# Optimization experiments

Hardware: AMD Instinct MI355X
Metric: run time of the kernel (lower is better)

## Reference

```python
import jax, jax.numpy as jnp
import numpy as np

N = 16                      # input_dim (state dimension)
EPS = 1e-6
TRIL_R, TRIL_C = np.tril_indices(N)   # 136 lower-triangular slots


def setup_inputs() -> dict:
    key = jax.random.key(0)
    ks = jax.random.split(key, 7)
    B = 131072
    def xavier(k, fan_in, fan_out):
        lim = float(np.sqrt(6.0 / (fan_in + fan_out)))
        return jax.random.uniform(k, (fan_in, fan_out), jnp.float32, -lim, lim)
    return {
        "points": jax.random.normal(ks[0], (B, N), jnp.float32),
        "W0": xavier(ks[1], N, 512),
        "b0": jax.random.normal(ks[2], (512,), jnp.float32) * 0.01,
        "W1": xavier(ks[3], 512, 512),
        "b1": jax.random.normal(ks[4], (512,), jnp.float32) * 0.01,
        "W2": xavier(ks[5], 512, 136),
        "b2": jax.random.normal(ks[6], (136,), jnp.float32) * 0.01,
    }


def reference(points, W0, b0, W1, b1, W2, b2):
    # MLP: tanh, tanh, identity
    h = jnp.tanh(points @ W0 + b0)
    h = jnp.tanh(h @ W1 + b1)
    net = h @ W2 + b2                         # [B, 136] tril entries
    B = points.shape[0]
    # Batched scatter into lower-triangular matrices M: [B, N, N]
    M = jnp.zeros((B, N, N), points.dtype).at[:, TRIL_R, TRIL_C].set(net)
    # x^T (M M^T) x == ||M^T x||^2
    y = jnp.einsum('bij,bi->bj', M, points)   # (M^T x)_j = sum_i M_ij x_i
    vals = jnp.sum(y * y, axis=-1) + EPS * jnp.sum(points * points, axis=-1)
    return vals.reshape(-1, 1)
```

## Files before the change

kernel.cpp:

```cpp
#include <hip/hip_runtime.h>

typedef __bf16 bf16x4 __attribute__((ext_vector_type(4)));
typedef __bf16 bf16x8 __attribute__((ext_vector_type(8)));
typedef float f32x16 __attribute__((ext_vector_type(16)));

#define W0F_OFF 0
#define W1F_OFF 8192
#define W2F_OFF (8192 + 262144)

__global__ void prep_weights(const float* __restrict__ W0,
                             const float* __restrict__ W1,
                             const float* __restrict__ W2,
                             __bf16* __restrict__ ws) {
    const int wave = blockIdx.x * 8 + (threadIdx.x >> 6);
    const int l   = threadIdx.x & 63;
    const int col = l & 31, kh = l >> 5;
    const float* src; int nt, kk, S, nlim;
    if (wave < 16)       { src = W0; nt = wave; kk = 0;          S = 512; nlim = 512; }
    else if (wave < 528) { int r = wave - 16;  src = W1; nt = r >> 5; kk = r & 31; S = 512; nlim = 512; }
    else                 { int r = wave - 528; src = W2; nt = r >> 5; kk = r & 31; S = 136; nlim = 136; }
    const int n  = nt * 32 + col;
    const int k0 = kk * 16 + kh * 8;
    bf16x8 v;
#pragma unroll
    for (int j = 0; j < 8; ++j)
        v[j] = (n < nlim) ? (__bf16)src[(k0 + j) * S + n] : (__bf16)0.0f;
    *(bf16x8*)(ws + wave * 512 + l * 8) = v;
}

__device__ __forceinline__ float fast_tanh(float x) {
#if __has_builtin(__builtin_amdgcn_exp2f)
    float e = __builtin_amdgcn_exp2f(x * 2.885390081777926f);
#else
    float e = exp2f(x * 2.885390081777926f);
#endif
    return 1.0f - 2.0f * __builtin_amdgcn_rcpf(e + 1.0f);
}

#define HSTR 520
#define NSTR 140

__global__ __launch_bounds__(512, 2)
void fused_mlp_quad(const float* __restrict__ points,
                    const float* __restrict__ b0,
                    const float* __restrict__ b1,
                    const float* __restrict__ b2,
                    const __bf16* __restrict__ ws,
                    float* __restrict__ out) {
    __shared__ __align__(16) unsigned char lds_raw[133120];
    __bf16* h  = (__bf16*)lds_raw;
    float* net = (float*)lds_raw;

    const __bf16* w0f = ws + W0F_OFF;
    const __bf16* w1f = ws + W1F_OFF;
    const __bf16* w2f = ws + W2F_OFF;

    const int tid = threadIdx.x;
    const int w   = tid >> 6;
    const int l   = tid & 63;
    const int ln  = l & 31;
    const int hi  = l >> 5;
    const int row0 = blockIdx.x * 128;

    const int lofs = l * 8;
    const int ofs16 = (blockIdx.x >> 3) & 15;

    const f32x16 fzero = {};


    auto PH0 = [&](int gb) {
        bf16x8 bx[2];
#pragma unroll
        for (int bt = 0; bt < 2; ++bt) {
            const float* src = points + (row0 + gb + bt * 32 + ln) * 16 + hi * 8;
            float4 p0 = ((const float4*)src)[0];
            float4 p1 = ((const float4*)src)[1];
            bf16x8 v;
            v[0] = (__bf16)p0.x; v[1] = (__bf16)p0.y; v[2] = (__bf16)p0.z; v[3] = (__bf16)p0.w;
            v[4] = (__bf16)p1.x; v[5] = (__bf16)p1.y; v[6] = (__bf16)p1.z; v[7] = (__bf16)p1.w;
            bx[bt] = v;
        }
#pragma unroll
        for (int t = 0; t < 2; ++t) {
            const int ntg = w * 2 + t;
            bf16x8 wf = *(const bf16x8*)(w0f + ntg * 512 + lofs);
#pragma unroll
            for (int bt = 0; bt < 2; ++bt) {
                f32x16 acc = {};
                acc = __builtin_amdgcn_mfma_f32_32x32x16_bf16(wf, bx[bt], acc, 0, 0, 0);
#pragma unroll
                for (int rg = 0; rg < 4; ++rg) {
                    const int n0 = ntg * 32 + 8 * rg + 4 * hi;
                    float4 bias = *(const float4*)(b0 + n0);
                    bf16x4 v;
                    v[0] = (__bf16)fast_tanh(acc[4 * rg + 0] + bias.x);
                    v[1] = (__bf16)fast_tanh(acc[4 * rg + 1] + bias.y);
                    v[2] = (__bf16)fast_tanh(acc[4 * rg + 2] + bias.z);
                    v[3] = (__bf16)fast_tanh(acc[4 * rg + 3] + bias.w);
                    *(bf16x4*)(h + (gb + bt * 32 + ln) * HSTR + n0) = v;
                }
            }
        }
    };

    auto P1M = [&](int gb, f32x16 (&acc1)[2][2]) {
#pragma unroll
        for (int bt = 0; bt < 2; ++bt)
#pragma unroll
            for (int t = 0; t < 2; ++t) acc1[bt][t] = fzero;
        const __bf16* arow0 = h + (gb + ln) * HSTR + hi * 8;
        const __bf16* arow1 = h + (gb + 32 + ln) * HSTR + hi * 8;
        const __bf16* wb0 = w1f + (w * 2 + 0) * 16384 + lofs;
        const __bf16* wb1 = w1f + (w * 2 + 1) * 16384 + lofs;
        for (int ks2 = 0; ks2 < 16; ++ks2) {
            const int ks = (ks2 + ofs16) & 15;
            bf16x8 aa[2][2], bb[2][2];
#pragma unroll
            for (int u = 0; u < 2; ++u) {
                const int kk = ks * 2 + u;
                aa[u][0] = *(const bf16x8*)(arow0 + kk * 16);
                aa[u][1] = *(const bf16x8*)(arow1 + kk * 16);
                bb[u][0] = *(const bf16x8*)(wb0 + kk * 512);
                bb[u][1] = *(const bf16x8*)(wb1 + kk * 512);
            }
#pragma unroll
            for (int u = 0; u < 2; ++u) {
#pragma unroll
                for (int t = 0; t < 2; ++t) {
                    acc1[0][t] = __builtin_amdgcn_mfma_f32_32x32x16_bf16(bb[u][t], aa[u][0], acc1[0][t], 0, 0, 0);
                    acc1[1][t] = __builtin_amdgcn_mfma_f32_32x32x16_bf16(bb[u][t], aa[u][1], acc1[1][t], 0, 0, 0);
                }
            }
        }
    };

    auto P1E = [&](int gb, f32x16 (&acc1)[2][2]) {
#pragma unroll
        for (int t = 0; t < 2; ++t)
#pragma unroll
            for (int bt = 0; bt < 2; ++bt)
#pragma unroll
                for (int rg = 0; rg < 4; ++rg) {
                    const int n0 = (w * 2 + t) * 32 + 8 * rg + 4 * hi;
                    float4 bias = *(const float4*)(b1 + n0);
                    bf16x4 v;
                    v[0] = (__bf16)fast_tanh(acc1[bt][t][4 * rg + 0] + bias.x);
                    v[1] = (__bf16)fast_tanh(acc1[bt][t][4 * rg + 1] + bias.y);
                    v[2] = (__bf16)fast_tanh(acc1[bt][t][4 * rg + 2] + bias.z);
                    v[3] = (__bf16)fast_tanh(acc1[bt][t][4 * rg + 3] + bias.w);
                    *(bf16x4*)(h + (gb + bt * 32 + ln) * HSTR + n0) = v;
                }
    };

    auto P2M = [&](int gb, f32x16 (&acc2)[2]) {
        acc2[0] = fzero; acc2[1] = fzero;
        if (w < 5) {
            const __bf16* arow0 = h + (gb + ln) * HSTR + hi * 8;
            const __bf16* arow1 = h + (gb + 32 + ln) * HSTR + hi * 8;
            const __bf16* wq = w2f + w * 16384 + lofs;
            for (int ks2 = 0; ks2 < 16; ++ks2) {
                const int ks = (ks2 + ofs16) & 15;
                bf16x8 wv[2], a0[2], a1[2];
#pragma unroll
                for (int u = 0; u < 2; ++u) {
                    const int kk = ks * 2 + u;
                    wv[u] = *(const bf16x8*)(wq + kk * 512);
                    a0[u] = *(const bf16x8*)(arow0 + kk * 16);
                    a1[u] = *(const bf16x8*)(arow1 + kk * 16);
                }
#pragma unroll
                for (int u = 0; u < 2; ++u) {
                    acc2[0] = __builtin_amdgcn_mfma_f32_32x32x16_bf16(wv[u], a0[u], acc2[0], 0, 0, 0);
                    acc2[1] = __builtin_amdgcn_mfma_f32_32x32x16_bf16(wv[u], a1[u], acc2[1], 0, 0, 0);
                }
            }
        }
    };

    auto P2E = [&](int gb, f32x16 (&acc2)[2]) {
        if (w < 5) {
#pragma unroll
            for (int bt = 0; bt < 2; ++bt)
#pragma unroll
                for (int rg = 0; rg < 4; ++rg) {
                    const int n0 = w * 32 + 8 * rg + 4 * hi;
                    if (n0 < 136) {
                        float4 bias = *(const float4*)(b2 + n0);
                        float4 v;
                        v.x = acc2[bt][4 * rg + 0] + bias.x;
                        v.y = acc2[bt][4 * rg + 1] + bias.y;
                        v.z = acc2[bt][4 * rg + 2] + bias.z;
                        v.w = acc2[bt][4 * rg + 3] + bias.w;
                        *(float4*)(net + (gb + bt * 32 + ln) * NSTR + n0) = v;
                    }
                }
        }
    };

    auto PH3 = [&](int gb) {
        const int r  = gb + (tid >> 3);
        const int jg = tid & 7;
        const float* xp = points + (row0 + r) * 16;
        float xv[16];
#pragma unroll
        for (int i = 0; i < 4; ++i) {
            float4 v = ((const float4*)xp)[i];
            xv[i * 4 + 0] = v.x; xv[i * 4 + 1] = v.y;
            xv[i * 4 + 2] = v.z; xv[i * 4 + 3] = v.w;
        }
        float sumsq = 0.f;
#pragma unroll
        for (int i = 0; i < 16; ++i) sumsq += xv[i] * xv[i];
        float p = 0.f;
#pragma unroll
        for (int jj = 0; jj < 2; ++jj) {
            const int j = jg + jj * 8;
            float y = 0.f;
#pragma unroll
            for (int i = 0; i < 16; ++i) {
                float mv = net[r * NSTR + ((i * (i + 1)) >> 1) + j];
                y += (i >= j) ? mv * xv[i] : 0.f;
            }
            p += y * y;
        }
        p += __shfl_xor(p, 1);
        p += __shfl_xor(p, 2);
        p += __shfl_xor(p, 4);
        if (jg == 0) out[row0 + r] = p + 1e-6f * sumsq;
    };

#define SEP asm volatile("" ::: "memory")

    f32x16 acc_a[2][2], acc_b[2][2], acc2_a[2], acc2_b[2];

    PH0(0);
    __syncthreads();
    if (w < 4) { P1M(0, acc_a); SEP; PH0(64); }
    else       { PH0(64); SEP; P1M(0, acc_a); }
    __syncthreads();
    if (w < 4) { P1M(64, acc_b); SEP; P1E(0, acc_a); }
    else       { P1E(0, acc_a); SEP; P1M(64, acc_b); }
    __syncthreads();
    if (w < 4) { P2M(0, acc2_a); SEP; P1E(64, acc_b); }
    else       { P1E(64, acc_b); SEP; P2M(0, acc2_a); }
    __syncthreads();
    if (w < 4) { P2M(64, acc2_b); SEP; P2E(0, acc2_a); }
    else       { P2E(0, acc2_a); SEP; P2M(64, acc2_b); }
    __syncthreads();
    P2E(64, acc2_b); SEP; PH3(0);
    __syncthreads();
    PH3(64);
#undef SEP
}

extern "C" void kernel_launch(void* const* d_in, const int* in_sizes, int n_in,
                              void* d_out, int out_size, void* d_ws, size_t ws_size,
                              hipStream_t stream) {
    const float* points = (const float*)d_in[0];
    const float* W0 = (const float*)d_in[1];
    const float* b0 = (const float*)d_in[2];
    const float* W1 = (const float*)d_in[3];
    const float* b1 = (const float*)d_in[4];
    const float* W2 = (const float*)d_in[5];
    const float* b2 = (const float*)d_in[6];
    __bf16* ws = (__bf16*)d_ws;
    float* out = (float*)d_out;

    prep_weights<<<86, 512, 0, stream>>>(W0, W1, W2, ws);

    const int B = in_sizes[0] / 16;
    fused_mlp_quad<<<B / 128, 512, 0, stream>>>(points, b0, b1, b2, ws, out);
}
```

Before: 203.2 us.

## Rebalance layer-2 MFMA work across all waves and fold tanh scale into weights

```diff
diff --git a/kernel.cpp b/kernel.cpp
--- a/kernel.cpp
+++ b/kernel.cpp
@@ -3,6 +3,8 @@
 typedef __bf16 bf16x4 __attribute__((ext_vector_type(4)));
 typedef __bf16 bf16x8 __attribute__((ext_vector_type(8)));
 typedef float f32x16 __attribute__((ext_vector_type(16)));
+
+#define TC 2.885390081777926f
 
 #define W0F_OFF 0
 #define W1F_OFF 8192
@@ -15,24 +17,24 @@
     const int wave = blockIdx.x * 8 + (threadIdx.x >> 6);
     const int l   = threadIdx.x & 63;
     const int col = l & 31, kh = l >> 5;
-    const float* src; int nt, kk, S, nlim;
-    if (wave < 16)       { src = W0; nt = wave; kk = 0;          S = 512; nlim = 512; }
-    else if (wave < 528) { int r = wave - 16;  src = W1; nt = r >> 5; kk = r & 31; S = 512; nlim = 512; }
-    else                 { int r = wave - 528; src = W2; nt = r >> 5; kk = r & 31; S = 136; nlim = 136; }
+    const float* src; int nt, kk, S, nlim; float scl;
+    if (wave < 16)       { src = W0; nt = wave; kk = 0;      S = 512; nlim = 512; scl = TC; }
+    else if (wave < 528) { int r = wave - 16;  src = W1; nt = r >> 5; kk = r & 31; S = 512; nlim = 512; scl = TC; }
+    else                 { int r = wave - 528; src = W2; nt = r >> 5; kk = r & 31; S = 136; nlim = 136; scl = 1.0f; }
     const int n  = nt * 32 + col;
     const int k0 = kk * 16 + kh * 8;
     bf16x8 v;
 #pragma unroll
     for (int j = 0; j < 8; ++j)
-        v[j] = (n < nlim) ? (__bf16)src[(k0 + j) * S + n] : (__bf16)0.0f;
+        v[j] = (n < nlim) ? (__bf16)(src[(k0 + j) * S + n] * scl) : (__bf16)0.0f;
     *(bf16x8*)(ws + wave * 512 + l * 8) = v;
 }
 
-__device__ __forceinline__ float fast_tanh(float x) {
+__device__ __forceinline__ float fast_tanh_pre(float y) {
 #if __has_builtin(__builtin_amdgcn_exp2f)
-    float e = __builtin_amdgcn_exp2f(x * 2.885390081777926f);
+    float e = __builtin_amdgcn_exp2f(y);
 #else
-    float e = exp2f(x * 2.885390081777926f);
+    float e = exp2f(y);
 #endif
     return 1.0f - 2.0f * __builtin_amdgcn_rcpf(e + 1.0f);
 }
@@ -64,193 +66,215 @@
 
     const int lofs = l * 8;
     const int ofs16 = (blockIdx.x >> 3) & 15;
+    const int ofs8  = (blockIdx.x >> 3) & 7;
+
+    const int nt2 = w >> 1;
+    const int bt2 = w & 1;
+    const bool two = (w < 2);
 
     const f32x16 fzero = {};
 
-
-    auto PH0 = [&](int gb) {
-        bf16x8 bx[2];
-#pragma unroll
-        for (int bt = 0; bt < 2; ++bt) {
-            const float* src = points + (row0 + gb + bt * 32 + ln) * 16 + hi * 8;
-            float4 p0 = ((const float4*)src)[0];
-            float4 p1 = ((const float4*)src)[1];
-            bf16x8 v;
-            v[0] = (__bf16)p0.x; v[1] = (__bf16)p0.y; v[2] = (__bf16)p0.z; v[3] = (__bf16)p0.w;
-            v[4] = (__bf16)p1.x; v[5] = (__bf16)p1.y; v[6] = (__bf16)p1.z; v[7] = (__bf16)p1.w;
-            bx[bt] = v;
-        }
-#pragma unroll
-        for (int t = 0; t < 2; ++t) {
-            const int ntg = w * 2 + t;
-            bf16x8 wf = *(const bf16x8*)(w0f + ntg * 512 + lofs);
-#pragma unroll
-            for (int bt = 0; bt < 2; ++bt) {
-                f32x16 acc = {};
-                acc = __builtin_amdgcn_mfma_f32_32x32x16_bf16(wf, bx[bt], acc, 0, 0, 0);
-#pragma unroll
-                for (int rg = 0; rg < 4; ++rg) {
-                    const int n0 = ntg * 32 + 8 * rg + 4 * hi;
-                    float4 bias = *(const float4*)(b0 + n0);
-                    bf16x4 v;
-                    v[0] = (__bf16)fast_tanh(acc[4 * rg + 0] + bias.x);
-                    v[1] = (__bf16)fast_tanh(acc[4 * rg + 1] + bias.y);
-                    v[2] = (__bf16)fast_tanh(acc[4 * rg + 2] + bias.z);
-                    v[3] = (__bf16)fast_tanh(acc[4 * rg + 3] + bias.w);
-                    *(bf16x4*)(h + (gb + bt * 32 + ln) * HSTR + n0) = v;
-                }
-            }
-        }
-    };
-
-    auto P1M = [&](int gb, f32x16 (&acc1)[2][2]) {
-#pragma unroll
-        for (int bt = 0; bt < 2; ++bt)
-#pragma unroll
-            for (int t = 0; t < 2; ++t) acc1[bt][t] = fzero;
-        const __bf16* arow0 = h + (gb + ln) * HSTR + hi * 8;
-        const __bf16* arow1 = h + (gb + 32 + ln) * HSTR + hi * 8;
-        const __bf16* wb0 = w1f + (w * 2 + 0) * 16384 + lofs;
-        const __bf16* wb1 = w1f + (w * 2 + 1) * 16384 + lofs;
-        for (int ks2 = 0; ks2 < 16; ++ks2) {
-            const int ks = (ks2 + ofs16) & 15;
-            bf16x8 aa[2][2], bb[2][2];
-#pragma unroll
-            for (int u = 0; u < 2; ++u) {
-                const int kk = ks * 2 + u;
-                aa[u][0] = *(const bf16x8*)(arow0 + kk * 16);
-                aa[u][1] = *(const bf16x8*)(arow1 + kk * 16);
-                bb[u][0] = *(const bf16x8*)(wb0 + kk * 512);
-                bb[u][1] = *(const bf16x8*)(wb1 + kk * 512);
-            }
-#pragma unroll
-            for (int u = 0; u < 2; ++u) {
-#pragma unroll
-                for (int t = 0; t < 2; ++t) {
-                    acc1[0][t] = __builtin_amdgcn_mfma_f32_32x32x16_bf16(bb[u][t], aa[u][0], acc1[0][t], 0, 0, 0);
-                    acc1[1][t] = __builtin_amdgcn_mfma_f32_32x32x16_bf16(bb[u][t], aa[u][1], acc1[1][t], 0, 0, 0);
-                }
-            }
-        }
-    };
-
-    auto P1E = [&](int gb, f32x16 (&acc1)[2][2]) {
-#pragma unroll
-        for (int t = 0; t < 2; ++t)
-#pragma unroll
-            for (int bt = 0; bt < 2; ++bt)
-#pragma unroll
-                for (int rg = 0; rg < 4; ++rg) {
-                    const int n0 = (w * 2 + t) * 32 + 8 * rg + 4 * hi;
-                    float4 bias = *(const float4*)(b1 + n0);
-                    bf16x4 v;
-                    v[0] = (__bf16)fast_tanh(acc1[bt][t][4 * rg + 0] + bias.x);
-                    v[1] = (__bf16)fast_tanh(acc1[bt][t][4 * rg + 1] + bias.y);
-                    v[2] = (__bf16)fast_tanh(acc1[bt][t][4 * rg + 2] + bias.z);
-                    v[3] = (__bf16)fast_tanh(acc1[bt][t][4 * rg + 3] + bias.w);
-                    *(bf16x4*)(h + (gb + bt * 32 + ln) * HSTR + n0) = v;
-                }
-    };
-
-    auto P2M = [&](int gb, f32x16 (&acc2)[2]) {
-        acc2[0] = fzero; acc2[1] = fzero;
-        if (w < 5) {
-            const __bf16* arow0 = h + (gb + ln) * HSTR + hi * 8;
-            const __bf16* arow1 = h + (gb + 32 + ln) * HSTR + hi * 8;
-            const __bf16* wq = w2f + w * 16384 + lofs;
-            for (int ks2 = 0; ks2 < 16; ++ks2) {
-                const int ks = (ks2 + ofs16) & 15;
-                bf16x8 wv[2], a0[2], a1[2];
-#pragma unroll
-                for (int u = 0; u < 2; ++u) {
-                    const int kk = ks * 2 + u;
-                    wv[u] = *(const bf16x8*)(wq + kk * 512);
-                    a0[u] = *(const bf16x8*)(arow0 + kk * 16);
-                    a1[u] = *(const bf16x8*)(arow1 + kk * 16);
-                }
-#pragma unroll
-                for (int u = 0; u < 2; ++u) {
-                    acc2[0] = __builtin_amdgcn_mfma_f32_32x32x16_bf16(wv[u], a0[u], acc2[0], 0, 0, 0);
-                    acc2[1] = __builtin_amdgcn_mfma_f32_32x32x16_bf16(wv[u], a1[u], acc2[1], 0, 0, 0);
-                }
-            }
-        }
-    };
-
-    auto P2E = [&](int gb, f32x16 (&acc2)[2]) {
-        if (w < 5) {
-#pragma unroll
-            for (int bt = 0; bt < 2; ++bt)
-#pragma unroll
-                for (int rg = 0; rg < 4; ++rg) {
-                    const int n0 = w * 32 + 8 * rg + 4 * hi;
-                    if (n0 < 136) {
-                        float4 bias = *(const float4*)(b2 + n0);
-                        float4 v;
-                        v.x = acc2[bt][4 * rg + 0] + bias.x;
-                        v.y = acc2[bt][4 * rg + 1] + bias.y;
-                        v.z = acc2[bt][4 * rg + 2] + bias.z;
-                        v.w = acc2[bt][4 * rg + 3] + bias.w;
-                        *(float4*)(net + (gb + bt * 32 + ln) * NSTR + n0) = v;
-                    }
-                }
-        }
-    };
-
-    auto PH3 = [&](int gb) {
-        const int r  = gb + (tid >> 3);
-        const int jg = tid & 7;
-        const float* xp = points + (row0 + r) * 16;
-        float xv[16];
-#pragma unroll
-        for (int i = 0; i < 4; ++i) {
-            float4 v = ((const float4*)xp)[i];
-            xv[i * 4 + 0] = v.x; xv[i * 4 + 1] = v.y;
-            xv[i * 4 + 2] = v.z; xv[i * 4 + 3] = v.w;
-        }
-        float sumsq = 0.f;
-#pragma unroll
-        for (int i = 0; i < 16; ++i) sumsq += xv[i] * xv[i];
-        float p = 0.f;
-#pragma unroll
-        for (int jj = 0; jj < 2; ++jj) {
-            const int j = jg + jj * 8;
-            float y = 0.f;
-#pragma unroll
-            for (int i = 0; i < 16; ++i) {
-                float mv = net[r * NSTR + ((i * (i + 1)) >> 1) + j];
-                y += (i >= j) ? mv * xv[i] : 0.f;
-            }
-            p += y * y;
-        }
-        p += __shfl_xor(p, 1);
-        p += __shfl_xor(p, 2);
-        p += __shfl_xor(p, 4);
-        if (jg == 0) out[row0 + r] = p + 1e-6f * sumsq;
-    };
-
+#define MFMA32(a, b, c) __builtin_amdgcn_mfma_f32_32x32x16_bf16(a, b, c, 0, 0, 0)
 #define SEP asm volatile("" ::: "memory")
 
-    f32x16 acc_a[2][2], acc_b[2][2], acc2_a[2], acc2_b[2];
+#define PH0(gb) do {                                                          \
+    bf16x8 bx0, bx1;                                                          \
+    {   const float* src = points + (row0 + (gb) + ln) * 16 + hi * 8;         \
+        float4 p0 = ((const float4*)src)[0], p1 = ((const float4*)src)[1];    \
+        bf16x8 v;                                                             \
+        v[0]=(__bf16)p0.x; v[1]=(__bf16)p0.y; v[2]=(__bf16)p0.z; v[3]=(__bf16)p0.w; \
+        v[4]=(__bf16)p1.x; v[5]=(__bf16)p1.y; v[6]=(__bf16)p1.z; v[7]=(__bf16)p1.w; \
+        bx0 = v; }                                                            \
+    {   const float* src = points + (row0 + (gb) + 32 + ln) * 16 + hi * 8;    \
+        float4 p0 = ((const float4*)src)[0], p1 = ((const float4*)src)[1];    \
+        bf16x8 v;                                                             \
+        v[0]=(__bf16)p0.x; v[1]=(__bf16)p0.y; v[2]=(__bf16)p0.z; v[3]=(__bf16)p0.w; \
+        v[4]=(__bf16)p1.x; v[5]=(__bf16)p1.y; v[6]=(__bf16)p1.z; v[7]=(__bf16)p1.w; \
+        bx1 = v; }                                                            \
+    _Pragma("unroll")                                                         \
+    for (int t = 0; t < 2; ++t) {                                             \
+        const int ntg = w * 2 + t;                                            \
+        bf16x8 wf = *(const bf16x8*)(w0f + ntg * 512 + lofs);                 \
+        f32x16 ac0 = {}, ac1 = {};                                            \
+        ac0 = MFMA32(wf, bx0, ac0);                                           \
+        ac1 = MFMA32(wf, bx1, ac1);                                           \
+        _Pragma("unroll")                                                     \
+        for (int rg = 0; rg < 4; ++rg) {                                      \
+            const int n0 = ntg * 32 + 8 * rg + 4 * hi;                        \
+            float4 bias = *(const float4*)(b0 + n0);                          \
+            bf16x4 v;                                                         \
+            v[0]=(__bf16)fast_tanh_pre(fmaf(TC,bias.x,ac0[4*rg+0]));          \
+            v[1]=(__bf16)fast_tanh_pre(fmaf(TC,bias.y,ac0[4*rg+1]));          \
+            v[2]=(__bf16)fast_tanh_pre(fmaf(TC,bias.z,ac0[4*rg+2]));          \
+            v[3]=(__bf16)fast_tanh_pre(fmaf(TC,bias.w,ac0[4*rg+3]));          \
+            *(bf16x4*)(h + ((gb) + ln) * HSTR + n0) = v;                      \
+            v[0]=(__bf16)fast_tanh_pre(fmaf(TC,bias.x,ac1[4*rg+0]));          \
+            v[1]=(__bf16)fast_tanh_pre(fmaf(TC,bias.y,ac1[4*rg+1]));          \
+            v[2]=(__bf16)fast_tanh_pre(fmaf(TC,bias.z,ac1[4*rg+2]));          \
+            v[3]=(__bf16)fast_tanh_pre(fmaf(TC,bias.w,ac1[4*rg+3]));          \
+            *(bf16x4*)(h + ((gb) + 32 + ln) * HSTR + n0) = v;                 \
+        }                                                                     \
+    }                                                                         \
+} while (0)
+
+#define P1M(gb, A00, A01, A10, A11) do {                                      \
+    A00 = fzero; A01 = fzero; A10 = fzero; A11 = fzero;                       \
+    const __bf16* arow0 = h + ((gb) + ln) * HSTR + hi * 8;                    \
+    const __bf16* arow1 = h + ((gb) + 32 + ln) * HSTR + hi * 8;               \
+    const __bf16* wb0 = w1f + (w * 2 + 0) * 16384 + lofs;                     \
+    const __bf16* wb1 = w1f + (w * 2 + 1) * 16384 + lofs;                     \
+    for (int ks2 = 0; ks2 < 16; ++ks2) {                                      \
+        const int ks = (ks2 + ofs16) & 15;                                    \
+        bf16x8 aa00, aa01, aa10, aa11, bb00, bb01, bb10, bb11;                \
+        {   const int kk = ks * 2;                                            \
+            aa00 = *(const bf16x8*)(arow0 + kk * 16);                         \
+            aa01 = *(const bf16x8*)(arow1 + kk * 16);                         \
+            bb00 = *(const bf16x8*)(wb0 + kk * 512);                          \
+            bb01 = *(const bf16x8*)(wb1 + kk * 512); }                        \
+        {   const int kk = ks * 2 + 1;                                        \
+            aa10 = *(const bf16x8*)(arow0 + kk * 16);                         \
+            aa11 = *(const bf16x8*)(arow1 + kk * 16);                         \
+            bb10 = *(const bf16x8*)(wb0 + kk * 512);                          \
+            bb11 = *(const bf16x8*)(wb1 + kk * 512); }                        \
+        A00 = MFMA32(bb00, aa00, A00);  A01 = MFMA32(bb01, aa00, A01);        \
+        A10 = MFMA32(bb00, aa01, A10);  A11 = MFMA32(bb01, aa01, A11);        \
+        A00 = MFMA32(bb10, aa10, A00);  A01 = MFMA32(bb11, aa10, A01);        \
+        A10 = MFMA32(bb10, aa11, A10);  A11 = MFMA32(bb11, aa11, A11);        \
+    }                                                                         \
+} while (0)
+
+#define P1E(gb, A00, A01, A10, A11) do {                                      \
+    _Pragma("unroll")                                                         \
+    for (int rg = 0; rg < 4; ++rg) {                                          \
+        const int n0a = (w * 2 + 0) * 32 + 8 * rg + 4 * hi;                   \
+        const int n0b = (w * 2 + 1) * 32 + 8 * rg + 4 * hi;                   \
+        float4 ba = *(const float4*)(b1 + n0a);                               \
+        float4 bb = *(const float4*)(b1 + n0b);                               \
+        bf16x4 v;                                                             \
+        v[0]=(__bf16)fast_tanh_pre(fmaf(TC,ba.x,A00[4*rg+0]));                \
+        v[1]=(__bf16)fast_tanh_pre(fmaf(TC,ba.y,A00[4*rg+1]));                \
+        v[2]=(__bf16)fast_tanh_pre(fmaf(TC,ba.z,A00[4*rg+2]));                \
+        v[3]=(__bf16)fast_tanh_pre(fmaf(TC,ba.w,A00[4*rg+3]));                \
+        *(bf16x4*)(h + ((gb) + ln) * HSTR + n0a) = v;                         \
+        v[0]=(__bf16)fast_tanh_pre(fmaf(TC,bb.x,A01[4*rg+0]));                \
+        v[1]=(__bf16)fast_tanh_pre(fmaf(TC,bb.y,A01[4*rg+1]));                \
+        v[2]=(__bf16)fast_tanh_pre(fmaf(TC,bb.z,A01[4*rg+2]));                \
+        v[3]=(__bf16)fast_tanh_pre(fmaf(TC,bb.w,A01[4*rg+3]));                \
+        *(bf16x4*)(h + ((gb) + ln) * HSTR + n0b) = v;                         \
+        v[0]=(__bf16)fast_tanh_pre(fmaf(TC,ba.x,A10[4*rg+0]));                \
+        v[1]=(__bf16)fast_tanh_pre(fmaf(TC,ba.y,A10[4*rg+1]));                \
+        v[2]=(__bf16)fast_tanh_pre(fmaf(TC,ba.z,A10[4*rg+2]));                \
+        v[3]=(__bf16)fast_tanh_pre(fmaf(TC,ba.w,A10[4*rg+3]));                \
+        *(bf16x4*)(h + ((gb) + 32 + ln) * HSTR + n0a) = v;                    \
+        v[0]=(__bf16)fast_tanh_pre(fmaf(TC,bb.x,A11[4*rg+0]));                \
+        v[1]=(__bf16)fast_tanh_pre(fmaf(TC,bb.y,A11[4*rg+1]));                \
+        v[2]=(__bf16)fast_tanh_pre(fmaf(TC,bb.z,A11[4*rg+2]));                \
+        v[3]=(__bf16)fast_tanh_pre(fmaf(TC,bb.w,A11[4*rg+3]));                \
+        *(bf16x4*)(h + ((gb) + 32 + ln) * HSTR + n0b) = v;                    \
+    }                                                                         \
+} while (0)
+
+#define P2M(gb, CA, CE) do {                                                  \
+    CA = fzero; CE = fzero;                                                   \
+    const __bf16* arowA = h + ((gb) + bt2 * 32 + ln) * HSTR + hi * 8;         \
+    const __bf16* arowE = h + ((gb) + (w & 1) * 32 + ln) * HSTR + hi * 8;     \
+    const __bf16* wbA = w2f + nt2 * 16384 + lofs;                             \
+    const __bf16* wbE = w2f + 4 * 16384 + lofs;                               \
+    for (int ks2 = 0; ks2 < 8; ++ks2) {                                       \
+        const int ks = (ks2 + ofs8) & 7;                                      \
+        bf16x8 aA0, wA0, aA1, wA1, aA2, wA2, aA3, wA3;                        \
+        bf16x8 aE0 = {}, wE0 = {}, aE1 = {}, wE1 = {}, aE2 = {}, wE2 = {}, aE3 = {}, wE3 = {}; \
+        {   const int kk = ks * 4;                                            \
+            aA0 = *(const bf16x8*)(arowA + kk * 16); wA0 = *(const bf16x8*)(wbA + kk * 512);       \
+            aA1 = *(const bf16x8*)(arowA + (kk+1)*16); wA1 = *(const bf16x8*)(wbA + (kk+1)*512);   \
+            aA2 = *(const bf16x8*)(arowA + (kk+2)*16); wA2 = *(const bf16x8*)(wbA + (kk+2)*512);   \
+            aA3 = *(const bf16x8*)(arowA + (kk+3)*16); wA3 = *(const bf16x8*)(wbA + (kk+3)*512);   \
+            if (two) {                                                        \
+                aE0 = *(const bf16x8*)(arowE + kk * 16); wE0 = *(const bf16x8*)(wbE + kk * 512);   \
+                aE1 = *(const bf16x8*)(arowE + (kk+1)*16); wE1 = *(const bf16x8*)(wbE + (kk+1)*512); \
+                aE2 = *(const bf16x8*)(arowE + (kk+2)*16); wE2 = *(const bf16x8*)(wbE + (kk+2)*512); \
+                aE3 = *(const bf16x8*)(arowE + (kk+3)*16); wE3 = *(const bf16x8*)(wbE + (kk+3)*512); \
+            } }                                                               \
+        CA = MFMA32(wA0, aA0, CA); CA = MFMA32(wA1, aA1, CA);                 \
+        CA = MFMA32(wA2, aA2, CA); CA = MFMA32(wA3, aA3, CA);                 \
+        if (two) {                                                            \
+            CE = MFMA32(wE0, aE0, CE); CE = MFMA32(wE1, aE1, CE);             \
+            CE = MFMA32(wE2, aE2, CE); CE = MFMA32(wE3, aE3, CE);             \
+        }                                                                     \
+    }                                                                         \
+} while (0)
+
+#define P2E(gb, CA, CE) do {                                                  \
+    _Pragma("unroll")                                                         \
+    for (int rg = 0; rg < 4; ++rg) {                                          \
+        const int n0 = nt2 * 32 + 8 * rg + 4 * hi;                            \
+        float4 bias = *(const float4*)(b2 + n0);                              \
+        float4 v;                                                             \
+        v.x = CA[4*rg+0] + bias.x; v.y = CA[4*rg+1] + bias.y;                 \
+        v.z = CA[4*rg+2] + bias.z; v.w = CA[4*rg+3] + bias.w;                 \
+        *(float4*)(net + ((gb) + bt2 * 32 + ln) * NSTR + n0) = v;             \
+    }                                                                         \
+    if (two) {                                                                \
+        const int n0 = 128 + 4 * hi;                                          \
+        float4 bias = *(const float4*)(b2 + n0);                              \
+        float4 v;                                                             \
+        v.x = CE[0] + bias.x; v.y = CE[1] + bias.y;                           \
+        v.z = CE[2] + bias.z; v.w = CE[3] + bias.w;                           \
+        *(float4*)(net + ((gb) + (w & 1) * 32 + ln) * NSTR + n0) = v;         \
+    }                                                                         \
+} while (0)
+
+#define PH3(gb) do {                                                          \
+    const int rl = tid >> 3;                                                  \
+    const int jg = tid & 7;                                                   \
+    const float* xp = points + (row0 + (gb) + rl) * 16;                       \
+    float xv[16];                                                             \
+    _Pragma("unroll")                                                         \
+    for (int i = 0; i < 4; ++i) {                                             \
+        float4 v = ((const float4*)xp)[i];                                    \
+        xv[i*4+0] = v.x; xv[i*4+1] = v.y; xv[i*4+2] = v.z; xv[i*4+3] = v.w;   \
+    }                                                                         \
+    float sumsq = 0.f;                                                        \
+    _Pragma("unroll")                                                         \
+    for (int i = 0; i < 16; ++i) sumsq += xv[i] * xv[i];                      \
+    float p = 0.f;                                                            \
+    _Pragma("unroll")                                                         \
+    for (int jj = 0; jj < 2; ++jj) {                                          \
+        const int j = jg + jj * 8;                                            \
+        float y = 0.f;                                                        \
+        _Pragma("unroll")                                                     \
+        for (int i = 0; i < 16; ++i) {                                        \
+            float mv = net[((gb) + rl) * NSTR + ((i * (i + 1)) >> 1) + j];    \
+            y += (i >= j) ? mv * xv[i] : 0.f;                                 \
+        }                                                                     \
+        p += y * y;                                                           \
+    }                                                                         \
+    p += __shfl_xor(p, 1);                                                    \
+    p += __shfl_xor(p, 2);                                                    \
+    p += __shfl_xor(p, 4);                                                    \
+    if (jg == 0) out[row0 + (gb) + rl] = p + 1e-6f * sumsq;                   \
+} while (0)
+
+    f32x16 a1A00, a1A01, a1A10, a1A11;
+    f32x16 a1B00, a1B01, a1B10, a1B11;
+    f32x16 c2aA, c2eA, c2aB, c2eB;
 
     PH0(0);
     __syncthreads();
-    if (w < 4) { P1M(0, acc_a); SEP; PH0(64); }
-    else       { PH0(64); SEP; P1M(0, acc_a); }
-    __syncthreads();
-    if (w < 4) { P1M(64, acc_b); SEP; P1E(0, acc_a); }
-    else       { P1E(0, acc_a); SEP; P1M(64, acc_b); }
-    __syncthreads();
-    if (w < 4) { P2M(0, acc2_a); SEP; P1E(64, acc_b); }
-    else       { P1E(64, acc_b); SEP; P2M(0, acc2_a); }
-    __syncthreads();
-    if (w < 4) { P2M(64, acc2_b); SEP; P2E(0, acc2_a); }
-    else       { P2E(0, acc2_a); SEP; P2M(64, acc2_b); }
-    __syncthreads();
-    P2E(64, acc2_b); SEP; PH3(0);
+    if (w < 4) { P1M(0, a1A00, a1A01, a1A10, a1A11); SEP; PH0(64); }
+    else       { PH0(64); SEP; P1M(0, a1A00, a1A01, a1A10, a1A11); }
+    __syncthreads();
+    if (w < 4) { P1M(64, a1B00, a1B01, a1B10, a1B11); SEP; P1E(0, a1A00, a1A01, a1A10, a1A11); }
+    else       { P1E(0, a1A00, a1A01, a1A10, a1A11); SEP; P1M(64, a1B00, a1B01, a1B10, a1B11); }
+    __syncthreads();
+    if (w < 4) { P2M(0, c2aA, c2eA); SEP; P1E(64, a1B00, a1B01, a1B10, a1B11); }
+    else       { P1E(64, a1B00, a1B01, a1B10, a1B11); SEP; P2M(0, c2aA, c2eA); }
+    __syncthreads();
+    P2M(64, c2aB, c2eB); SEP; P2E(0, c2aA, c2eA);
+    __syncthreads();
+    PH3(0); SEP; P2E(64, c2aB, c2eB);
     __syncthreads();
     PH3(64);
-#undef SEP
 }
 
 extern "C" void kernel_launch(void* const* d_in, const int* in_sizes, int n_in,
```

Result: no change. 200.3 us (-1.4%).
